# Performance work log

Measured on AMD Instinct MI355X. Metric: run time of the kernel, lower is better.

Reference implementation:

```python
import jax, jax.numpy as jnp
import numpy as np
from jax import lax

C = 128; G = 8; K = 3; P = K * K; GC = C // G
N, H, W = 4, 96, 96
EPS = 1e-5

def conv_bn_silu(x, w, gamma, beta, rmean, rvar, stride, pad):
    # Conv2d(bias=False) + BatchNorm2d(eval) + SiLU, NCHW
    y = lax.conv_general_dilated(x, w, (stride, stride), [(pad, pad), (pad, pad)],
                                 dimension_numbers=('NCHW', 'OIHW', 'NCHW'))
    s = gamma / jnp.sqrt(rvar + EPS)
    y = y * s[None, :, None, None] + (beta - rmean * s)[None, :, None, None]
    return y * jax.nn.sigmoid(y)

def dcnv3(x, dw_w, dw_b, ln_g, ln_b, off_w, off_b, m_w, m_b, ip_w, ip_b, op_w, op_b):
    # InternImage DCNv3, channels-last input (N,H,W,C), k=3 s=1 pad=1 dil=1 group=G, offset_scale=1
    n, h, w, c = x.shape
    xp = x @ ip_w.T + ip_b  # input_proj
    # offset/mask branch: depthwise 3x3 conv + LayerNorm + GELU on the ORIGINAL input
    dw = lax.conv_general_dilated(x, dw_w, (1, 1), [(1, 1), (1, 1)],
                                  dimension_numbers=('NHWC', 'HWIO', 'NHWC'),
                                  feature_group_count=c) + dw_b
    dw = (dw - dw.mean(-1, keepdims=True)) / jnp.sqrt(dw.var(-1, keepdims=True) + EPS) * ln_g + ln_b
    dw = jax.nn.gelu(dw)
    off = (dw @ off_w.T + off_b).reshape(n, h, w, G, P, 2)  # (..., (dx, dy))
    m = jax.nn.softmax((dw @ m_w.T + m_b).reshape(n, h, w, G, P), -1)
    pad = 1
    hp, wp = h + 2 * pad, w + 2 * pad
    xpad = jnp.pad(xp, ((0, 0), (pad, pad), (pad, pad), (0, 0))).reshape(n, hp, wp, G, GC)
    ky, kx = jnp.meshgrid(jnp.arange(-1, 2, dtype=x.dtype), jnp.arange(-1, 2, dtype=x.dtype), indexing='ij')
    # absolute sampling coords in padded image (grid_sample align_corners=False equivalent)
    py = (jnp.arange(h, dtype=x.dtype) + pad)[None, :, None, None, None] + ky.reshape(-1) + off[..., 1]
    px = (jnp.arange(w, dtype=x.dtype) + pad)[None, None, :, None, None] + kx.reshape(-1) + off[..., 0]
    yf = jnp.floor(py); xf = jnp.floor(px)
    wy = py - yf; wx = px - xf
    y0 = yf.astype(jnp.int32); x0 = xf.astype(jnp.int32)
    n_idx = jnp.arange(n)[:, None, None, None, None]
    g_idx = jnp.arange(G)[None, None, None, :, None]

    def gat(yi, xi):
        valid = ((yi >= 0) & (yi < hp) & (xi >= 0) & (xi < wp)).astype(x.dtype)
        v = xpad[n_idx, jnp.clip(yi, 0, hp - 1), jnp.clip(xi, 0, wp - 1), g_idx]  # (n,h,w,G,P,GC)
        return v * valid[..., None]

    v = (gat(y0, x0) * ((1 - wy) * (1 - wx))[..., None]
         + gat(y0, x0 + 1) * ((1 - wy) * wx)[..., None]
         + gat(y0 + 1, x0) * (wy * (1 - wx))[..., None]
         + gat(y0 + 1, x0 + 1) * (wy * wx)[..., None])
    out = jnp.einsum('nhwgpc,nhwgp->nhwgc', v, m).reshape(n, h, w, c)
    return out @ op_w.T + op_b  # output_proj

def _forward(x0, x1, x2, conv_w, conv_g, conv_b, conv_rm, conv_rv,
             conv1_w, conv1_g, conv1_b, conv1_rm, conv1_rv,
             conv2_w, conv2_g, conv2_b, conv2_rm, conv2_rv,
             dw_w, dw_b, ln_g, ln_b, off_w, off_b, m_w, m_b, ip_w, ip_b, op_w, op_b):
    n, _, h, w = x0.shape
    # x1: 256 ch > 128 -> self.conv (1x1); smaller spatial -> bilinear upsample to HW
    y1 = conv_bn_silu(x1, conv_w, conv_g, conv_b, conv_rm, conv_rv, 1, 0)
    feat_up1 = jax.image.resize(y1, (n, C, h, w), method='bilinear')
    # x2: 64 ch < 128 -> self.conv1 (1x1); larger spatial -> self.conv2 (3x3 s2) to HW
    y2 = conv_bn_silu(x2, conv1_w, conv1_g, conv1_b, conv1_rm, conv1_rv, 1, 0)
    feat_up2 = conv_bn_silu(y2, conv2_w, conv2_g, conv2_b, conv2_rm, conv2_rv, 2, 1)
    d1 = dcnv3(feat_up1.transpose(0, 2, 3, 1), dw_w, dw_b, ln_g, ln_b, off_w, off_b, m_w, m_b, ip_w, ip_b, op_w, op_b)
    d2 = dcnv3(feat_up2.transpose(0, 2, 3, 1), dw_w, dw_b, ln_g, ln_b, off_w, off_b, m_w, m_b, ip_w, ip_b, op_w, op_b)
    a1 = jax.nn.relu(d1).transpose(0, 3, 1, 2)
    a2 = jax.nn.relu(d2).transpose(0, 3, 1, 2)
    return jnp.concatenate([a1, x0, a2], axis=1)  # (N, 3C, H, W)

def setup_inputs():
    ks = jax.random.split(jax.random.key(0), 24)
    f = jnp.float32
    return {
        'x0': jax.random.normal(ks[0], (N, C, H, W), f),
        'x1': jax.random.normal(ks[1], (N, 2 * C, H // 2, W // 2), f),
        'x2': jax.random.normal(ks[2], (N, C // 2, 2 * H, 2 * W), f),
        'conv_w': jax.random.normal(ks[3], (C, 2 * C, 1, 1), f) * 0.05,
        'conv_g': jnp.ones((C,), f), 'conv_b': jnp.zeros((C,), f),
        'conv_rm': jax.random.normal(ks[4], (C,), f) * 0.1,
        'conv_rv': jax.random.uniform(ks[5], (C,), f) + 0.5,
        'conv1_w': jax.random.normal(ks[6], (C, C // 2, 1, 1), f) * 0.08,
        'conv1_g': jnp.ones((C,), f), 'conv1_b': jnp.zeros((C,), f),
        'conv1_rm': jax.random.normal(ks[7], (C,), f) * 0.1,
        'conv1_rv': jax.random.uniform(ks[8], (C,), f) + 0.5,
        'conv2_w': jax.random.normal(ks[9], (C, C, 3, 3), f) * 0.03,
        'conv2_g': jnp.ones((C,), f), 'conv2_b': jnp.zeros((C,), f),
        'conv2_rm': jax.random.normal(ks[10], (C,), f) * 0.1,
        'conv2_rv': jax.random.uniform(ks[11], (C,), f) + 0.5,
        'dw_w': jax.random.normal(ks[12], (3, 3, 1, C), f) * 0.1,
        'dw_b': jnp.zeros((C,), f),
        'ln_g': jnp.ones((C,), f), 'ln_b': jnp.zeros((C,), f),
        'off_w': jax.random.normal(ks[13], (G * P * 2, C), f) * 0.01,
        'off_b': jnp.zeros((G * P * 2,), f),
        'm_w': jax.random.normal(ks[14], (G * P, C), f) * 0.05,
        'm_b': jnp.zeros((G * P,), f),
        'ip_w': jax.random.normal(ks[15], (C, C), f) * 0.05,
        'ip_b': jnp.zeros((C,), f),
        'op_w': jax.random.normal(ks[16], (C, C), f) * 0.05,
        'op_b': jnp.zeros((C,), f),
    }

def reference(x0, x1, x2, conv_w, conv_g, conv_b, conv_rm, conv_rv,
              conv1_w, conv1_g, conv1_b, conv1_rm, conv1_rv,
              conv2_w, conv2_g, conv2_b, conv2_rm, conv2_rv,
              dw_w, dw_b, ln_g, ln_b, off_w, off_b, m_w, m_b, ip_w, ip_b, op_w, op_b):
    return _forward(x0, x1, x2, conv_w, conv_g, conv_b, conv_rm, conv_rv,
                    conv1_w, conv1_g, conv1_b, conv1_rm, conv1_rv,
                    conv2_w, conv2_g, conv2_b, conv2_rm, conv2_rv,
                    dw_w, dw_b, ln_g, ln_b, off_w, off_b, m_w, m_b, ip_w, ip_b, op_w, op_b)
```

## Files before the change

### kernel.cpp

```cpp
#include <hip/hip_runtime.h>
#include <cstdint>
#include <cstddef>

#define EPSV 1e-5f
#define NPIX 9216
#define LDA 136
#define LDK 72

typedef __bf16 bf16;
typedef _Float16 f16;
typedef __attribute__((ext_vector_type(8))) __bf16 bf16x8;
typedef __attribute__((ext_vector_type(4))) __bf16 bf16x4;
typedef __attribute__((ext_vector_type(2))) _Float16 f16x2;
typedef __attribute__((ext_vector_type(4))) float  f32x4;

__device__ __forceinline__ float silu_f(float v) { return v / (1.f + __expf(-v)); }

__global__ __launch_bounds__(256) void prep_kernel(
    const float* __restrict__ conv_w, const float* __restrict__ conv_g,
    const float* __restrict__ conv_b, const float* __restrict__ conv_rm, const float* __restrict__ conv_rv,
    const float* __restrict__ conv1_w, const float* __restrict__ conv1_g,
    const float* __restrict__ conv1_b, const float* __restrict__ conv1_rm, const float* __restrict__ conv1_rv,
    const float* __restrict__ conv2_w, const float* __restrict__ conv2_g,
    const float* __restrict__ conv2_bb, const float* __restrict__ conv2_rm, const float* __restrict__ conv2_rv,
    const float* __restrict__ ip_w, const float* __restrict__ op_w,
    const float* __restrict__ off_w, const float* __restrict__ m_w,
    const float* __restrict__ off_b, const float* __restrict__ m_b,
    float* __restrict__ WTSf, bf16* __restrict__ WTSb)
{
  int idx = blockIdx.x * 256 + threadIdx.x;
  if (idx < 608) {
    if (idx < 128) {
      int co = idx;
      float s = conv_g[co] * rsqrtf(conv_rv[co] + EPSV);
      WTSf[idx] = conv_b[co] - conv_rm[co] * s;
    } else if (idx < 256) {
      int co = idx - 128;
      float s = conv1_g[co] * rsqrtf(conv1_rv[co] + EPSV);
      WTSf[idx] = conv1_b[co] - conv1_rm[co] * s;
    } else if (idx < 384) {
      int co = idx - 256;
      float s = conv2_g[co] * rsqrtf(conv2_rv[co] + EPSV);
      WTSf[idx] = conv2_bb[co] - conv2_rm[co] * s;
    } else {
      int col = idx - 384;
      WTSf[idx] = (col < 144) ? off_b[col] : (col < 216 ? m_b[col - 144] : 0.f);
    }
  } else {
    int j = idx - 608;
    if (j < 32768) {
      int co = j >> 8, ci = j & 255;
      float s = conv_g[co] * rsqrtf(conv_rv[co] + EPSV);
      WTSb[j] = (bf16)(conv_w[co * 256 + ci] * s);
    } else if (j < 40960) {
      int r = j - 32768; int co = r >> 6, ci = r & 63;
      float s = conv1_g[co] * rsqrtf(conv1_rv[co] + EPSV);
      WTSb[j] = (bf16)(conv1_w[co * 64 + ci] * s);
    } else if (j < 188416) {
      int r = j - 40960; int kp = r >> 14; int rr = r & 16383;
      int co = rr >> 7, ci = rr & 127;
      float s = conv2_g[co] * rsqrtf(conv2_rv[co] + EPSV);
      WTSb[j] = (bf16)(conv2_w[(co * 128 + ci) * 9 + kp] * s);
    } else if (j < 204800) {
      int r = j - 188416; int co = r >> 7, ci = r & 127;
      WTSb[j] = (bf16)ip_w[co * 128 + ci];
    } else if (j < 233472) {
      int r = j - 204800; int co = r >> 7, ci = r & 127;
      float v = (co < 144) ? off_w[co * 128 + ci] : (co < 216 ? m_w[(co - 144) * 128 + ci] : 0.f);
      WTSb[j] = (bf16)v;
    } else if (j < 249856) {
      int r = j - 233472; int co = r >> 7, ci = r & 127;
      WTSb[j] = (bf16)op_w[co * 128 + ci];
    }
  }
}

__global__ __launch_bounds__(256) void c1x1_mfma_kernel(
    const float* __restrict__ x, const bf16* __restrict__ W,
    const float* __restrict__ bias, int K, int HW, bf16* __restrict__ outb)
{
  __shared__ bf16 As[64 * LDK];
  __shared__ bf16 Bs[128 * LDK];
  int m0 = blockIdx.x << 6;
  int t = threadIdx.x;
  int n = m0 / HW; int hw0 = m0 - n * HW;
  const float* xn = x + (size_t)n * K * HW;
  int wv = t >> 6, lane = t & 63;
  int lrow = lane & 15, q = lane >> 4;
  int n0 = wv * 32;
  f32x4 acc[4][2];
#pragma unroll
  for (int i = 0; i < 4; ++i)
#pragma unroll
    for (int j = 0; j < 2; ++j)
#pragma unroll
      for (int e = 0; e < 4; ++e) acc[i][j][e] = 0.f;

  for (int k0 = 0; k0 < K; k0 += 64) {
    if (k0) __syncthreads();
    for (int i = t; i < 1024; i += 256) {
      int px = i & 63; int ci4 = (i >> 6) << 2;
      bf16x4 p;
#pragma unroll
      for (int j = 0; j < 4; ++j)
        p[j] = (bf16)xn[(size_t)(k0 + ci4 + j) * HW + hw0 + px];
      *(bf16x4*)&As[px * LDK + ci4] = p;
    }
    for (int i = t; i < 1024; i += 256) {
      int co = i >> 3; int k8 = (i & 7) << 3;
      *(bf16x8*)&Bs[co * LDK + k8] = *(const bf16x8*)&W[(size_t)co * K + k0 + k8];
    }
    __syncthreads();
#pragma unroll
    for (int ks = 0; ks < 2; ++ks) {
      int ko = ks * 32 + q * 8;
      bf16x8 bfr0 = *(const bf16x8*)&Bs[(n0 + lrow) * LDK + ko];
      bf16x8 bfr1 = *(const bf16x8*)&Bs[(n0 + 16 + lrow) * LDK + ko];
#pragma unroll
      for (int mi = 0; mi < 4; ++mi) {
        bf16x8 afr = *(const bf16x8*)&As[(mi * 16 + lrow) * LDK + ko];
        acc[mi][0] = __builtin_amdgcn_mfma_f32_16x16x32_bf16(afr, bfr0, acc[mi][0], 0, 0, 0);
        acc[mi][1] = __builtin_amdgcn_mfma_f32_16x16x32_bf16(afr, bfr1, acc[mi][1], 0, 0, 0);
      }
    }
  }
#pragma unroll
  for (int mi = 0; mi < 4; ++mi) {
#pragma unroll
    for (int nj = 0; nj < 2; ++nj) {
      int co = n0 + nj * 16 + lrow;
      float bb = bias[co];
#pragma unroll
      for (int r = 0; r < 4; ++r) {
        int m = m0 + mi * 16 + q * 4 + r;
        outb[(size_t)m * 128 + co] = (bf16)silu_f(acc[mi][nj][r] + bb);
      }
    }
  }
}

__global__ __launch_bounds__(256) void upsample_kernel(
    const bf16* __restrict__ y1b, bf16* __restrict__ feat1b)
{
  int idx = blockIdx.x * 256 + threadIdx.x;
  int c4 = (idx & 31) << 2;
  int pw = idx >> 5;
  int ow = pw % 96; int t1 = pw / 96;
  int oh = t1 % 96; int n = t1 / 96;
  float sh = oh * 0.5f - 0.25f, sw = ow * 0.5f - 0.25f;
  float hf = floorf(sh), wf = floorf(sw);
  float fy = sh - hf, fx = sw - wf;
  int h0 = (int)hf, w0 = (int)wf;
  int h0c = max(h0, 0), h1c = min(h0 + 1, 47);
  int w0c = max(w0, 0), w1c = min(w0 + 1, 47);
  const bf16* yn = y1b + (size_t)n * 2304 * 128 + c4;
  bf16x4 v00 = *(const bf16x4*)&yn[(h0c * 48 + w0c) * 128];
  bf16x4 v01 = *(const bf16x4*)&yn[(h0c * 48 + w1c) * 128];
  bf16x4 v10 = *(const bf16x4*)&yn[(h1c * 48 + w0c) * 128];
  bf16x4 v11 = *(const bf16x4*)&yn[(h1c * 48 + w1c) * 128];
  bf16x4 o;
#pragma unroll
  for (int e = 0; e < 4; ++e) {
    float v = (1.f - fy) * ((1.f - fx) * (float)v00[e] + fx * (float)v01[e])
            + fy * ((1.f - fx) * (float)v10[e] + fx * (float)v11[e]);
    o[e] = (bf16)v;
  }
  *(bf16x4*)&feat1b[((size_t)n * NPIX + oh * 96 + ow) * 128 + c4] = o;
}

__global__ __launch_bounds__(256) void conv2_mfma_kernel(
    const bf16* __restrict__ y2b, const bf16* __restrict__ W2b,
    const float* __restrict__ b2, bf16* __restrict__ feat2b)
{
  __shared__ bf16 As[64 * LDA];
  __shared__ bf16 Bs[128 * LDA];
  int m0 = blockIdx.x << 6;
  int t = threadIdx.x;
  int wv = t >> 6, lane = t & 63;
  int lrow = lane & 15, q = lane >> 4;
  int n0 = wv * 32;
  f32x4 acc[4][2];
#pragma unroll
  for (int i = 0; i < 4; ++i)
#pragma unroll
    for (int j = 0; j < 2; ++j)
#pragma unroll
      for (int e = 0; e < 4; ++e) acc[i][j][e] = 0.f;
  bf16x8 zv;
#pragma unroll
  for (int e = 0; e < 8; ++e) zv[e] = (bf16)0.f;

  for (int kp = 0; kp < 9; ++kp) {
    int kh = kp / 3, kw = kp - kh * 3;
    __syncthreads();
    for (int i = t; i < 1024; i += 256) {
      int row = i >> 4; int c8 = (i & 15) << 3;
      int m = m0 + row;
      int nimg = m / NPIX; int hw = m - nimg * NPIX;
      int oh = hw / 96, ow = hw - oh * 96;
      int ih = 2 * oh - 1 + kh, iw = 2 * ow - 1 + kw;
      bf16x8 v = zv;
      if ((unsigned)ih < 192u && (unsigned)iw < 192u)
        v = *(const bf16x8*)&y2b[(((size_t)nimg * 192 + ih) * 192 + iw) * 128 + c8];
      *(bf16x8*)&As[row * LDA + c8] = v;
    }
    const bf16* Wk = W2b + kp * 16384;
    for (int i = t; i < 2048; i += 256) {
      int nn = i >> 4; int k8 = (i & 15) << 3;
      *(bf16x8*)&Bs[nn * LDA + k8] = *(const bf16x8*)&Wk[nn * 128 + k8];
    }
    __syncthreads();
#pragma unroll
    for (int ks = 0; ks < 4; ++ks) {
      bf16x8 bfr0 = *(const bf16x8*)&Bs[(n0 + lrow) * LDA + ks * 32 + q * 8];
      bf16x8 bfr1 = *(const bf16x8*)&Bs[(n0 + 16 + lrow) * LDA + ks * 32 + q * 8];
#pragma unroll
      for (int mi = 0; mi < 4; ++mi) {
        bf16x8 afr = *(const bf16x8*)&As[(mi * 16 + lrow) * LDA + ks * 32 + q * 8];
        acc[mi][0] = __builtin_amdgcn_mfma_f32_16x16x32_bf16(afr, bfr0, acc[mi][0], 0, 0, 0);
        acc[mi][1] = __builtin_amdgcn_mfma_f32_16x16x32_bf16(afr, bfr1, acc[mi][1], 0, 0, 0);
      }
    }
  }
#pragma unroll
  for (int mi = 0; mi < 4; ++mi) {
#pragma unroll
    for (int nj = 0; nj < 2; ++nj) {
      int co = n0 + nj * 16 + lrow;
      float bb = b2[co];
#pragma unroll
      for (int r = 0; r < 4; ++r) {
        int m = m0 + mi * 16 + q * 4 + r;
        feat2b[(size_t)m * 128 + co] = (bf16)silu_f(acc[mi][nj][r] + bb);
      }
    }
  }
}

__global__ __launch_bounds__(256) void mm_bf16_kernel(
    const bf16* __restrict__ A, const bf16* __restrict__ W,
    const float* __restrict__ bias, int Nc, int ostride, int act,
    int store_mode, void* __restrict__ outp)
{
  __shared__ bf16 As[64 * LDA];
  __shared__ bf16 Bs[128 * LDA];
  int m0 = blockIdx.x << 6;
  int nb = blockIdx.y << 7;
  int cols_here = Nc - nb; if (cols_here > 128) cols_here = 128;
  int t = threadIdx.x;
  for (int i = t; i < 1024; i += 256) {
    int row = i >> 4; int c8 = (i & 15) << 3;
    *(bf16x8*)&As[row * LDA + c8] = *(const bf16x8*)&A[(size_t)(m0 + row) * 128 + c8];
  }
  bf16x8 zv;
#pragma unroll
  for (int e = 0; e < 8; ++e) zv[e] = (bf16)0.f;
  for (int i = t; i < 2048; i += 256) {
    int n = i >> 4; int k8 = (i & 15) << 3;
    bf16x8 v = (n < cols_here) ? *(const bf16x8*)&W[(size_t)(nb + n) * 128 + k8] : zv;
    *(bf16x8*)&Bs[n * LDA + k8] = v;
  }
  __syncthreads();

  int wv = t >> 6, lane = t & 63;
  int lrow = lane & 15, q = lane >> 4;
  int n0 = wv * 32;
  f32x4 acc[4][2];
#pragma unroll
  for (int i = 0; i < 4; ++i)
#pragma unroll
    for (int j = 0; j < 2; ++j)
#pragma unroll
      for (int e = 0; e < 4; ++e) acc[i][j][e] = 0.f;

#pragma unroll
  for (int ks = 0; ks < 4; ++ks) {
    bf16x8 bfr0 = *(const bf16x8*)&Bs[(n0 + lrow) * LDA + ks * 32 + q * 8];
    bf16x8 bfr1 = *(const bf16x8*)&Bs[(n0 + 16 + lrow) * LDA + ks * 32 + q * 8];
#pragma unroll
    for (int mi = 0; mi < 4; ++mi) {
      bf16x8 afr = *(const bf16x8*)&As[(mi * 16 + lrow) * LDA + ks * 32 + q * 8];
      acc[mi][0] = __builtin_amdgcn_mfma_f32_16x16x32_bf16(afr, bfr0, acc[mi][0], 0, 0, 0);
      acc[mi][1] = __builtin_amdgcn_mfma_f32_16x16x32_bf16(afr, bfr1, acc[mi][1], 0, 0, 0);
    }
  }

  float* outf = (float*)outp;
  bf16*  outb = (bf16*)outp;
  f16*   outh = (f16*)outp;
#pragma unroll
  for (int mi = 0; mi < 4; ++mi) {
#pragma unroll
    for (int nj = 0; nj < 2; ++nj) {
      int col = nb + n0 + nj * 16 + lrow;
      if (col >= Nc) continue;
      float bb = bias[col];
#pragma unroll
      for (int r = 0; r < 4; ++r) {
        int m = m0 + mi * 16 + q * 4 + r;
        float v = acc[mi][nj][r] + bb;
        if (act == 1) v = fmaxf(v, 0.f);
        if (store_mode == 0) {
          outf[(size_t)m * ostride + col] = v;
        } else if (store_mode == 2) {
          outb[(size_t)m * 128 + col] = (bf16)v;
        } else if (store_mode == 3) {
          outh[(size_t)m * ostride + col] = (f16)v;
        } else {
          int nn = m / NPIX; int hw = m - nn * NPIX;
          int img = nn & 3; int choff = (nn >= 4) ? 256 : 0;
          outf[((size_t)(img * 384 + choff + col)) * NPIX + hw] = v;
        }
      }
    }
  }
}

__global__ __launch_bounds__(256) void dwln_kernel(
    const bf16* __restrict__ featb, const float* __restrict__ dw_w,
    const float* __restrict__ dw_b, const float* __restrict__ ln_g,
    const float* __restrict__ ln_b, bf16* __restrict__ dwgb)
{
  __shared__ float Wts[1152];
  __shared__ float Pb[384];
  int t = threadIdx.x;
  for (int i = t; i < 1152; i += 256) Wts[i] = dw_w[i];
  for (int i = t; i < 384; i += 256)
    Pb[i] = (i < 128) ? dw_b[i] : (i < 256 ? ln_g[i - 128] : ln_b[i - 256]);
  __syncthreads();

  int pxl = t >> 4;
  int c8 = (t & 15) << 3;
  int bid = blockIdx.x;
  int wg = (bid & 7) * 576 + (bid >> 3);
  int pixel = wg * 16 + pxl;
  int n = pixel / NPIX; int hw = pixel - n * NPIX;
  int h = hw / 96; int w = hw - h * 96;
  const bf16* fn = featb + (size_t)n * NPIX * 128 + c8;
  bf16x8 zv;
#pragma unroll
  for (int e = 0; e < 8; ++e) zv[e] = (bf16)0.f;

  bf16x8 v[9];
#pragma unroll
  for (int p = 0; p < 9; ++p) {
    int hh = h + p / 3 - 1, ww = w + (p % 3) - 1;
    bool valid = ((unsigned)hh < 96u) && ((unsigned)ww < 96u);
    int hc = min(max(hh, 0), 95), wc = min(max(ww, 0), 95);
    bf16x8 x = *(const bf16x8*)&fn[(hc * 96 + wc) * 128];
    v[p] = valid ? x : zv;
  }

  float acc[8];
#pragma unroll
  for (int e = 0; e < 8; ++e) acc[e] = Pb[c8 + e];
#pragma unroll
  for (int p = 0; p < 9; ++p) {
    f32x4 w0 = *(const f32x4*)&Wts[p * 128 + c8];
    f32x4 w1 = *(const f32x4*)&Wts[p * 128 + c8 + 4];
#pragma unroll
    for (int e = 0; e < 4; ++e) {
      acc[e]     += (float)v[p][e]     * w0[e];
      acc[4 + e] += (float)v[p][4 + e] * w1[e];
    }
  }

  float s = 0.f, qs = 0.f;
#pragma unroll
  for (int e = 0; e < 8; ++e) { s += acc[e]; qs += acc[e] * acc[e]; }
#pragma unroll
  for (int off = 8; off > 0; off >>= 1) {
    s  += __shfl_xor(s, off);
    qs += __shfl_xor(qs, off);
  }
  float mean = s * (1.f / 128.f);
  float var = qs * (1.f / 128.f) - mean * mean;
  float rstd = rsqrtf(var + EPSV);
  bf16x8 o;
#pragma unroll
  for (int e = 0; e < 8; ++e) {
    float xn = (acc[e] - mean) * rstd * Pb[128 + c8 + e] + Pb[256 + c8 + e];
    float z = 0.7978845608028654f * (xn + 0.044715f * xn * xn * xn);
    float th;
    if (z > 15.f) th = 1.f;
    else if (z < -15.f) th = -1.f;
    else { float e2 = __expf(2.f * z); th = (e2 - 1.f) / (e2 + 1.f); }
    o[e] = (bf16)(0.5f * xn * (1.f + th));
  }
  *(bf16x8*)&dwgb[(size_t)pixel * 128 + c8] = o;
}

__global__ __launch_bounds__(256, 6) void sample_kernel(
    const bf16* __restrict__ xpb, const f16* __restrict__ offm,
    bf16* __restrict__ vaggb)
{
  __shared__ uint32_t Sd[16 * 112];
  __shared__ float Pm[16 * 72];
  const f16* S = (const f16*)Sd;
  int t = threadIdx.x;
  int bid = blockIdx.x;
  int wg = (bid & 7) * 576 + (bid >> 3);
  {
    const uint32_t* src = (const uint32_t*)(offm + (size_t)wg * 16 * 224);
    for (int i = t; i < 1792; i += 256) Sd[i] = src[i];
  }
  __syncthreads();
  if (t < 128) {
    int px = t >> 3, gg = t & 7;
    const f16* L = S + px * 224 + 144 + gg * 9;
    float l[9]; float mx = -1e30f;
#pragma unroll
    for (int p = 0; p < 9; ++p) { l[p] = (float)L[p]; mx = fmaxf(mx, l[p]); }
    float se = 0.f;
#pragma unroll
    for (int p = 0; p < 9; ++p) { l[p] = __expf(l[p] - mx); se += l[p]; }
    float inv = 1.f / se;
    float* Pp = Pm + px * 72 + gg * 9;
#pragma unroll
    for (int p = 0; p < 9; ++p) Pp[p] = l[p] * inv;
  }
  __syncthreads();
  int pxl = t >> 4;
  int tid16 = t & 15;
  int g = tid16 >> 1;
  int c8 = (tid16 & 1) << 3;
  int pixel = wg * 16 + pxl;
  int n = pixel / NPIX; int hw = pixel - n * NPIX;
  int h = hw / 96; int w = hw - h * 96;
  const f16* Sp = S + pxl * 224 + g * 18;
  const float* Pp = Pm + pxl * 72 + g * 9;
  const bf16* xpn = xpb + (size_t)n * NPIX * 128 + g * 16 + c8;
  float acc[8];
#pragma unroll
  for (int e = 0; e < 8; ++e) acc[e] = 0.f;
#pragma unroll 1
  for (int kh = 0; kh < 3; ++kh) {
#pragma unroll
    for (int kw = 0; kw < 3; ++kw) {
      int p = kh * 3 + kw;
      f16x2 d2 = *(const f16x2*)&Sp[p * 2];
      float dx = (float)d2.x, dy = (float)d2.y;
      float pyu = (float)(h + kh - 1) + dy;
      float pxu = (float)(w + kw - 1) + dx;
      float yf = floorf(pyu), xf = floorf(pxu);
      float wy = pyu - yf, wx = pxu - xf;
      int y0 = (int)yf, x0 = (int)xf;
      float ay0 = ((unsigned)y0 < 96u) ? (1.f - wy) : 0.f;
      float ay1 = ((unsigned)(y0 + 1) < 96u) ? wy : 0.f;
      float ax0 = ((unsigned)x0 < 96u) ? (1.f - wx) : 0.f;
      float ax1 = ((unsigned)(x0 + 1) < 96u) ? wx : 0.f;
      int y0c = min(max(y0, 0), 95), y1c = min(max(y0 + 1, 0), 95);
      int x0c = min(max(x0, 0), 95), x1c = min(max(x0 + 1, 0), 95);
      float mp = Pp[p];
      float w00 = ay0 * ax0 * mp, w01 = ay0 * ax1 * mp;
      float w10 = ay1 * ax0 * mp, w11 = ay1 * ax1 * mp;
      bf16x8 v00 = *(const bf16x8*)&xpn[(y0c * 96 + x0c) * 128];
      bf16x8 v01 = *(const bf16x8*)&xpn[(y0c * 96 + x1c) * 128];
      bf16x8 v10 = *(const bf16x8*)&xpn[(y1c * 96 + x0c) * 128];
      bf16x8 v11 = *(const bf16x8*)&xpn[(y1c * 96 + x1c) * 128];
#pragma unroll
      for (int e = 0; e < 8; ++e) {
        acc[e] += w00 * (float)v00[e] + w01 * (float)v01[e]
                + w10 * (float)v10[e] + w11 * (float)v11[e];
      }
    }
  }
  bf16x8 o;
#pragma unroll
  for (int e = 0; e < 8; ++e) o[e] = (bf16)acc[e];
  *(bf16x8*)&vaggb[(size_t)pixel * 128 + g * 16 + c8] = o;
}

__global__ __launch_bounds__(256) void copy_x0_kernel(
    const float4* __restrict__ x0, float4* __restrict__ out)
{
  int idx = blockIdx.x * 256 + threadIdx.x;
  int n = idx / (128 * 2304);
  int r = idx - n * (128 * 2304);
  out[(size_t)(n * 384 + 128) * 2304 + r] = x0[(size_t)n * 128 * 2304 + r];
}

extern "C" void kernel_launch(void* const* d_in, const int* in_sizes, int n_in,
                              void* d_out, int out_size, void* d_ws, size_t ws_size,
                              hipStream_t stream)
{
  (void)in_sizes; (void)n_in; (void)out_size; (void)ws_size;
  const float* x0      = (const float*)d_in[0];
  const float* x1      = (const float*)d_in[1];
  const float* x2      = (const float*)d_in[2];
  const float* conv_w  = (const float*)d_in[3];
  const float* conv_g  = (const float*)d_in[4];
  const float* conv_b  = (const float*)d_in[5];
  const float* conv_rm = (const float*)d_in[6];
  const float* conv_rv = (const float*)d_in[7];
  const float* conv1_w = (const float*)d_in[8];
  const float* conv1_g = (const float*)d_in[9];
  const float* conv1_b = (const float*)d_in[10];
  const float* conv1_rm= (const float*)d_in[11];
  const float* conv1_rv= (const float*)d_in[12];
  const float* conv2_w = (const float*)d_in[13];
  const float* conv2_g = (const float*)d_in[14];
  const float* conv2_b = (const float*)d_in[15];
  const float* conv2_rm= (const float*)d_in[16];
  const float* conv2_rv= (const float*)d_in[17];
  const float* dw_w    = (const float*)d_in[18];
  const float* dw_b    = (const float*)d_in[19];
  const float* ln_g    = (const float*)d_in[20];
  const float* ln_b    = (const float*)d_in[21];
  const float* off_w   = (const float*)d_in[22];
  const float* off_b   = (const float*)d_in[23];
  const float* m_w     = (const float*)d_in[24];
  const float* m_b     = (const float*)d_in[25];
  const float* ip_w    = (const float*)d_in[26];
  const float* ip_b    = (const float*)d_in[27];
  const float* op_w    = (const float*)d_in[28];
  const float* op_b    = (const float*)d_in[29];
  float* out = (float*)d_out;
  char* WS = (char*)d_ws;

  bf16* featb  = (bf16*)WS;
  bf16* feat1b = featb;
  bf16* feat2b = featb + 4718592;
  bf16* y2b    = (bf16*)(WS + 18874368);
  bf16* xpb    = (bf16*)(WS + 18874368);
  bf16* dwgb   = (bf16*)(WS + 37748736);
  bf16* vaggb  = dwgb;
  bf16* y1b    = (bf16*)(WS + 56623104);
  f16*  offm   = (f16*)(WS + 58982400);
  float* WTSf  = (float*)(WS + 125042688);
  bf16*  WTSb  = (bf16*)(WS + 125045120);

  float* b1f  = WTSf;
  float* b1bf = WTSf + 128;
  float* b2f  = WTSf + 256;
  float* bomf = WTSf + 384;
  bf16* W1b  = WTSb;
  bf16* W1bb = WTSb + 32768;
  bf16* W2b  = WTSb + 40960;
  bf16* Wipb = WTSb + 188416;
  bf16* Womb = WTSb + 204800;
  bf16* Wopb = WTSb + 233472;

  prep_kernel<<<979, 256, 0, stream>>>(
      conv_w, conv_g, conv_b, conv_rm, conv_rv,
      conv1_w, conv1_g, conv1_b, conv1_rm, conv1_rv,
      conv2_w, conv2_g, conv2_b, conv2_rm, conv2_rv,
      ip_w, op_w, off_w, m_w, off_b, m_b, WTSf, WTSb);

  c1x1_mfma_kernel<<<144, 256, 0, stream>>>(x1, W1b, b1f, 256, 2304, y1b);
  upsample_kernel<<<4608, 256, 0, stream>>>(y1b, feat1b);

  c1x1_mfma_kernel<<<2304, 256, 0, stream>>>(x2, W1bb, b1bf, 64, 36864, y2b);
  conv2_mfma_kernel<<<576, 256, 0, stream>>>(y2b, W2b, b2f, feat2b);

  mm_bf16_kernel<<<dim3(1152, 1), 256, 0, stream>>>(featb, Wipb, ip_b, 128, 128, 0, 2, xpb);
  dwln_kernel<<<4608, 256, 0, stream>>>(featb, dw_w, dw_b, ln_g, ln_b, dwgb);
  mm_bf16_kernel<<<dim3(1152, 2), 256, 0, stream>>>(dwgb, Womb, bomf, 224, 224, 0, 3, offm);
  sample_kernel<<<4608, 256, 0, stream>>>(xpb, offm, vaggb);
  mm_bf16_kernel<<<dim3(1152, 1), 256, 0, stream>>>(vaggb, Wopb, op_b, 128, 0, 1, 1, out);

  copy_x0_kernel<<<4608, 256, 0, stream>>>((const float4*)x0, (float4*)out);
}
```

Baseline: 400.8 us.

## Fuse output projection GEMM into deformable sampling kernel epilogue

The sampling kernel now keeps its 16-pixel aggregated tile in shared memory and runs the 128x128 output projection with MFMA inside the same block. It then writes bias+ReLU results straight to the NCHW output, so the separate projection GEMM launch is gone. This removes the vagg intermediate's global write and read plus one kernel launch. In exchange it adds shared memory and an extra sync, may lower occupancy, and reads Wop from global per block while the output stores are strided per channel.

```diff
diff --git a/kernel.cpp b/kernel.cpp
--- a/kernel.cpp
+++ b/kernel.cpp
@@ -392,10 +392,12 @@
 
 __global__ __launch_bounds__(256, 6) void sample_kernel(
     const bf16* __restrict__ xpb, const f16* __restrict__ offm,
-    bf16* __restrict__ vaggb)
+    const bf16* __restrict__ Wop, const float* __restrict__ op_b,
+    float* __restrict__ out)
 {
   __shared__ uint32_t Sd[16 * 112];
   __shared__ float Pm[16 * 72];
+  __shared__ bf16 Avs[16 * LDA];
   const f16* S = (const f16*)Sd;
   int t = threadIdx.x;
   int bid = blockIdx.x;
@@ -468,7 +470,42 @@
   bf16x8 o;
 #pragma unroll
   for (int e = 0; e < 8; ++e) o[e] = (bf16)acc[e];
-  *(bf16x8*)&vaggb[(size_t)pixel * 128 + g * 16 + c8] = o;
+  *(bf16x8*)&Avs[pxl * LDA + g * 16 + c8] = o;
+  __syncthreads();
+
+  {
+    int wv = t >> 6, lane = t & 63;
+    int lrow = lane & 15, q = lane >> 4;
+    int n0 = wv * 32;
+    f32x4 pacc[2];
+#pragma unroll
+    for (int j = 0; j < 2; ++j)
+#pragma unroll
+      for (int e = 0; e < 4; ++e) pacc[j][e] = 0.f;
+#pragma unroll
+    for (int ks = 0; ks < 4; ++ks) {
+      int ko = ks * 32 + q * 8;
+      bf16x8 afr  = *(const bf16x8*)&Avs[lrow * LDA + ko];
+      bf16x8 bfr0 = *(const bf16x8*)&Wop[(size_t)(n0 + lrow) * 128 + ko];
+      bf16x8 bfr1 = *(const bf16x8*)&Wop[(size_t)(n0 + 16 + lrow) * 128 + ko];
+      pacc[0] = __builtin_amdgcn_mfma_f32_16x16x32_bf16(afr, bfr0, pacc[0], 0, 0, 0);
+      pacc[1] = __builtin_amdgcn_mfma_f32_16x16x32_bf16(afr, bfr1, pacc[1], 0, 0, 0);
+    }
+    int nn = (wg * 16) / NPIX;
+    int hwb = wg * 16 - nn * NPIX;
+    int img = nn & 3; int choff = (nn >= 4) ? 256 : 0;
+#pragma unroll
+    for (int nj = 0; nj < 2; ++nj) {
+      int col = n0 + nj * 16 + lrow;
+      float bb = op_b[col];
+      float* oc = out + ((size_t)(img * 384 + choff + col)) * NPIX + hwb;
+#pragma unroll
+      for (int r = 0; r < 4; ++r) {
+        int px = q * 4 + r;
+        oc[px] = fmaxf(pacc[nj][r] + bb, 0.f);
+      }
+    }
+  }
 }
 
 __global__ __launch_bounds__(256) void copy_x0_kernel(
@@ -524,7 +561,6 @@
   bf16* y2b    = (bf16*)(WS + 18874368);
   bf16* xpb    = (bf16*)(WS + 18874368);
   bf16* dwgb   = (bf16*)(WS + 37748736);
-  bf16* vaggb  = dwgb;
   bf16* y1b    = (bf16*)(WS + 56623104);
   f16*  offm   = (f16*)(WS + 58982400);
   float* WTSf  = (float*)(WS + 125042688);
@@ -556,8 +592,7 @@
   mm_bf16_kernel<<<dim3(1152, 1), 256, 0, stream>>>(featb, Wipb, ip_b, 128, 128, 0, 2, xpb);
   dwln_kernel<<<4608, 256, 0, stream>>>(featb, dw_w, dw_b, ln_g, ln_b, dwgb);
   mm_bf16_kernel<<<dim3(1152, 2), 256, 0, stream>>>(dwgb, Womb, bomf, 224, 224, 0, 3, offm);
-  sample_kernel<<<4608, 256, 0, stream>>>(xpb, offm, vaggb);
-  mm_bf16_kernel<<<dim3(1152, 1), 256, 0, stream>>>(vaggb, Wopb, op_b, 128, 0, 1, 1, out);
+  sample_kernel<<<4608, 256, 0, stream>>>(xpb, offm, Wopb, op_b, out);
 
   copy_x0_kernel<<<4608, 256, 0, stream>>>((const float4*)x0, (float4*)out);
 }
```

After: 384.0 us. -4.2%, faster.
